# Kernel optimization log

Measured on AMD Instinct MI355X. Metric: run time of the kernel, lower is better.

The kernel has to match this reference:

```python
import jax, jax.numpy as jnp
import numpy as np

N_WIRES = 16
VAR_DEPTH = 2
BATCH = 16


def _param_sizes():
    sizes = []
    n = N_WIRES
    lay = 0
    while n > 1:
        sizes.append(4 * int(np.ceil(N_WIRES / 2 ** lay)) * VAR_DEPTH)
        n = (n + 1) // 2
        lay += 1
    return sizes  # [128, 64, 32, 16]


def _apply_1q(psi, gate, w):
    # psi: (B, 2, ..., 2); gate: (2,2) complex; wire w lives on axis w+1
    psi = jnp.moveaxis(psi, w + 1, -1)
    psi = jnp.einsum('...j,ij->...i', psi, gate)
    return jnp.moveaxis(psi, -1, w + 1)


def _rx(psi, th, w):
    c = jnp.cos(th / 2).astype(jnp.complex64)
    s = jnp.sin(th / 2).astype(jnp.complex64)
    gate = jnp.stack([jnp.stack([c, -1j * s]), jnp.stack([-1j * s, c])])
    return _apply_1q(psi, gate, w)


def _rz(psi, th, w):
    ph = jnp.exp(0.5j * th * jnp.array([-1.0, 1.0], jnp.float32)).astype(jnp.complex64)
    shape = [1] * psi.ndim
    shape[w + 1] = 2
    return psi * ph.reshape(shape)


def _rzz(psi, th, wa, wb):
    # diag(e^{-i t/2}, e^{i t/2}, e^{i t/2}, e^{-i t/2}) -> sign = -1 if bits equal else +1
    sgn = jnp.array([[-1.0, 1.0], [1.0, -1.0]], jnp.float32)
    ph = jnp.exp(0.5j * th * sgn).astype(jnp.complex64)  # symmetric, transpose-safe
    a, b = min(wa, wb) + 1, max(wa, wb) + 1
    shape = [1] * psi.ndim
    shape[a] = 2
    shape[b] = 2
    return psi * ph.reshape(shape)


def _cnot(psi, c, t):
    p0 = jax.lax.slice_in_dim(psi, 0, 1, axis=c + 1)
    p1 = jax.lax.slice_in_dim(psi, 1, 2, axis=c + 1)
    return jnp.concatenate([p0, jnp.flip(p1, axis=t + 1)], axis=c + 1)


def _conv_layer(psi, params, active):
    n = len(active)
    for d in range(VAR_DEPTH):
        for j in range(n):
            base = 4 * j + d * 4 * n
            psi = _rx(psi, params[base + 0], active[j])
            psi = _rz(psi, params[base + 1], active[j])
            psi = _rx(psi, params[base + 2], active[j])
        for bg in (0, 1):
            for j in range(bg, n, 2):
                jn = (j + 1) % n  # ring coupling (wraps last->first)
                base = 4 * j + d * 4 * n
                psi = _rzz(psi, params[base + 3], active[j], active[jn])
    return psi


def _pool(psi, active):
    for j in range(0, len(active), 2):
        if j + 1 < len(active):
            psi = _cnot(psi, active[j], active[j + 1])
    return psi, active[::2]


def _forward(psi, params_list):
    active = list(range(N_WIRES))
    for p in params_list:
        psi = _conv_layer(psi, p, active)
        if len(active) > 1:
            psi, active = _pool(psi, active)
    w = active[0]  # measure Z on the surviving wire (wire 0)
    prob = psi.real ** 2 + psi.imag ** 2
    axes = tuple(a for a in range(1, psi.ndim) if a != w + 1)
    p2 = prob.sum(axis=axes)  # (B, 2)
    return p2[:, 0] - p2[:, 1]


def setup_inputs() -> dict:
    key = jax.random.key(0)
    ks = jax.random.split(key, 8)
    dim = 2 ** N_WIRES
    x_re = jax.random.normal(ks[0], (BATCH, dim), dtype=jnp.float32)
    x_im = jax.random.normal(ks[1], (BATCH, dim), dtype=jnp.float32)
    nrm = jnp.sqrt(jnp.sum(x_re ** 2 + x_im ** 2, axis=1, keepdims=True))
    x_re = x_re / nrm
    x_im = x_im / nrm
    sizes = _param_sizes()
    two_pi = 2.0 * np.pi
    params = [jax.random.uniform(ks[2 + i], (sizes[i],), dtype=jnp.float32) * two_pi
              for i in range(len(sizes))]
    return {"x_re": x_re, "x_im": x_im,
            "params0": params[0], "params1": params[1],
            "params2": params[2], "params3": params[3]}


def reference(x_re, x_im, params0, params1, params2, params3):
    psi = (x_re + 1j * x_im).astype(jnp.complex64)
    psi = psi.reshape((BATCH,) + (2,) * N_WIRES)
    return _forward(psi, [params0, params1, params2, params3])
```

## Files before the change

### kernel.cpp

```cpp
#include <hip/hip_runtime.h>


#define DEV __device__ __forceinline__

__device__ static const unsigned char G_CP[60] = {
  15,14,13,12,11,10,9,8,7,6,5,4,3,2,1,0,
  15,14,13,12,11,10,9,8,7,6,5,4,3,2,1,0,
  15,13,11,9,7,5,3,1,
  15,13,11,9,7,5,3,1,
  15,11,7,3,
  15,11,7,3,
  15,7,
  15,7
};
__device__ static const unsigned char G_CQ[60] = {
  14,13,12,11,10,9,8,7,6,5,4,3,2,1,0,15,
  14,13,12,11,10,9,8,7,6,5,4,3,2,1,0,15,
  13,11,9,7,5,3,1,15,
  13,11,9,7,5,3,1,15,
  11,7,3,15,
  11,7,3,15,
  7,15,
  7,15
};

DEV float2 F2(float x, float y){ float2 r; r.x = x; r.y = y; return r; }
DEV float2 cmulf(float2 a, float2 b){ return F2(a.x*b.x - a.y*b.y, a.x*b.y + a.y*b.x); }
DEV int swz(int j){ return j ^ ((j>>4)&15) ^ ((j>>8)&15); }

template<int B>
DEV void gate(float2* a, const float* __restrict__ g){
  float2 u00=F2(g[0],g[1]), u01=F2(g[2],g[3]), u10=F2(g[4],g[5]), u11=F2(g[6],g[7]);
  #pragma unroll
  for (int m=0; m<8; m++){
    int i0 = ((m>>B)<<(B+1)) | (m & ((1<<B)-1));
    int i1 = i0 | (1<<B);
    float2 x0=a[i0], x1=a[i1];
    a[i0] = F2(u00.x*x0.x - u00.y*x0.y + u01.x*x1.x - u01.y*x1.y,
               u00.x*x0.y + u00.y*x0.x + u01.x*x1.y + u01.y*x1.x);
    a[i1] = F2(u10.x*x0.x - u10.y*x0.y + u11.x*x1.x - u11.y*x1.y,
               u10.x*x0.y + u10.y*x0.x + u11.x*x1.y + u11.y*x1.x);
  }
}

template<int CB,int TB>
DEV void cnotg(float2* a){
  #pragma unroll
  for (int r=0; r<16; r++){
    if ( ((r>>CB)&1)==1 && ((r>>TB)&1)==0 ){
      float2 tmp = a[r]; a[r] = a[r | (1<<TB)]; a[r | (1<<TB)] = tmp;
    }
  }
}

template<int C0,int N,unsigned M0,unsigned M1,unsigned M2,unsigned M3>
DEV void diag(float2* a, const float* __restrict__ tbl, unsigned Ib){
  const unsigned regmask = M0|M1|M2|M3;
  float2 F0 = F2(1.f, 0.f);
  #pragma unroll
  for (int k=0; k<N; k++){
    const int p = G_CP[C0+k], q = G_CQ[C0+k];
    if ( !(((1u<<p)|(1u<<q)) & regmask) ){
      float c = tbl[480 + 2*(C0+k)], s = tbl[481 + 2*(C0+k)];
      unsigned x = ((Ib>>p) ^ (Ib>>q)) & 1u;
      F0 = cmulf(F0, F2(c, x ? s : -s));
    }
  }
  #pragma unroll
  for (int r=0; r<16; r++){
    unsigned Ir = Ib ^ ((r&1)?M0:0u) ^ ((r&2)?M1:0u) ^ ((r&4)?M2:0u) ^ ((r&8)?M3:0u);
    float2 ph = F0;
    #pragma unroll
    for (int k=0; k<N; k++){
      const int p = G_CP[C0+k], q = G_CQ[C0+k];
      if ( ((1u<<p)|(1u<<q)) & regmask ){
        float c = tbl[480 + 2*(C0+k)], s = tbl[481 + 2*(C0+k)];
        unsigned x = ((Ir>>p) ^ (Ir>>q)) & 1u;
        ph = cmulf(ph, F2(c, x ? s : -s));
      }
    }
    a[r] = cmulf(a[r], ph);
  }
}

__global__ void k_setup(const float* __restrict__ p0, const float* __restrict__ p1,
                        const float* __restrict__ p2, const float* __restrict__ p3,
                        float* __restrict__ tbl){
  int g = threadIdx.x;
  if (g >= 60) return;
  int d, j, n; const float* P;
  if (g < 32)      { n=16; d=(g>>4)&1; j=g&15; P=p0; }
  else if (g < 48) { n=8;  d=(g>>3)&1; j=g&7;  P=p1; }
  else if (g < 56) { n=4;  d=(g>>2)&1; j=g&3;  P=p2; }
  else             { n=2;  d=(g>>1)&1; j=g&1;  P=p3; }
  int base = 4*j + 4*n*d;
  double th0 = P[base+0], th1 = P[base+1], th2 = P[base+2], th3 = P[base+3];
  double c0 = cos(th0*0.5), s0 = sin(th0*0.5);
  double ca = cos(th1*0.5), sa = sin(th1*0.5);
  double c2 = cos(th2*0.5), s2 = sin(th2*0.5);
  double B00r =  ca*c0, B00i = -sa*c0;
  double B01r = -sa*s0, B01i = -ca*s0;
  double B10r =  sa*s0, B10i = -ca*s0;
  double B11r =  ca*c0, B11i =  sa*c0;
  double U00r = c2*B00r + s2*B10i, U00i = c2*B00i - s2*B10r;
  double U01r = c2*B01r + s2*B11i, U01i = c2*B01i - s2*B11r;
  double U10r = s2*B00i + c2*B10r, U10i = -s2*B00r + c2*B10i;
  double U11r = s2*B01i + c2*B11r, U11i = -s2*B01r + c2*B11i;
  float* o = tbl + g*8;
  o[0]=(float)U00r; o[1]=(float)U00i; o[2]=(float)U01r; o[3]=(float)U01i;
  o[4]=(float)U10r; o[5]=(float)U10i; o[6]=(float)U11r; o[7]=(float)U11i;
  tbl[480 + 2*g] = (float)cos(th3*0.5);
  tbl[481 + 2*g] = (float)sin(th3*0.5);
}

__global__ __launch_bounds__(256) void k_pass1(const float* __restrict__ xre, const float* __restrict__ xim,
                                               const float* __restrict__ tbl, float2* __restrict__ st){
  const int t = threadIdx.x;
  const int batch = blockIdx.x >> 4, o = blockIdx.x & 15;
  const unsigned hi = ((unsigned)batch<<16) | ((unsigned)o<<12);
  __shared__ float2 lds[2][4096];
  float2 a[16];
  #pragma unroll
  for (int rh=0; rh<4; rh++){
    unsigned I = hi | ((unsigned)t<<2) | ((unsigned)rh<<10);
    float4 re = *(const float4*)(xre + I);
    float4 im = *(const float4*)(xim + I);
    a[rh*4+0]=F2(re.x,im.x); a[rh*4+1]=F2(re.y,im.y);
    a[rh*4+2]=F2(re.z,im.z); a[rh*4+3]=F2(re.w,im.w);
  }
  gate<0>(a, tbl+15*8); gate<1>(a, tbl+14*8); gate<2>(a, tbl+5*8); gate<3>(a, tbl+4*8);
  #pragma unroll
  for (int r=0;r<16;r++){ int j = (r&3) | (t<<2) | ((r>>2)<<10); lds[0][swz(j)] = a[r]; }
  __syncthreads();
  #pragma unroll
  for (int r=0;r<16;r++){ int j = (t&3) | (r<<2) | ((t>>2)<<6); a[r] = lds[0][swz(j)]; }
  gate<0>(a, tbl+13*8); gate<1>(a, tbl+12*8); gate<2>(a, tbl+11*8); gate<3>(a, tbl+10*8);
  #pragma unroll
  for (int r=0;r<16;r++){ int j = (t&3) | (r<<2) | ((t>>2)<<6); lds[1][swz(j)] = a[r]; }
  __syncthreads();
  #pragma unroll
  for (int r=0;r<16;r++){ int j = (t&63) | (r<<6) | ((t>>6)<<10); a[r] = lds[1][swz(j)]; }
  gate<0>(a, tbl+9*8); gate<1>(a, tbl+8*8); gate<2>(a, tbl+7*8); gate<3>(a, tbl+6*8);
  #pragma unroll
  for (int r=0;r<16;r++){ int j = (t&63) | (r<<6) | ((t>>6)<<10); st[hi | j] = a[r]; }
}

__global__ __launch_bounds__(256) void k_pass2(const float* __restrict__ tbl, float2* __restrict__ st){
  const int t = threadIdx.x;
  const int batch = blockIdx.x >> 4, o = blockIdx.x & 15;
  const unsigned bb = (unsigned)batch<<16;
  __shared__ float2 lds[2][4096];
  float2 a[16];
  #pragma unroll
  for (int r=0;r<16;r++){
    unsigned I = (unsigned)(t&63) | ((unsigned)o<<6) | (((unsigned)(t>>6)&3u)<<10) | ((unsigned)r<<12) | bb;
    a[r] = st[I];
  }
  gate<0>(a, tbl+3*8); gate<1>(a, tbl+2*8); gate<2>(a, tbl+1*8); gate<3>(a, tbl+0*8);
  {
    unsigned Ib = (unsigned)(t&63) | ((unsigned)o<<6) | (((unsigned)(t>>6)&3u)<<10);
    diag<0,16, (1u<<12),(1u<<13),(1u<<14),(1u<<15)>(a, tbl, Ib);
  }
  gate<0>(a, tbl+19*8); gate<1>(a, tbl+18*8); gate<2>(a, tbl+17*8); gate<3>(a, tbl+16*8);
  #pragma unroll
  for (int r=0;r<16;r++){ int j = t | (r<<8); lds[0][swz(j)] = a[r]; }
  __syncthreads();
  #pragma unroll
  for (int r=0;r<16;r++){ int j = r | (t<<4); a[r] = lds[0][swz(j)]; }
  gate<0>(a, tbl+31*8); gate<1>(a, tbl+30*8); gate<2>(a, tbl+29*8); gate<3>(a, tbl+28*8);
  #pragma unroll
  for (int r=0;r<16;r++){ int j = r | (t<<4); lds[1][swz(j)] = a[r]; }
  __syncthreads();
  #pragma unroll
  for (int r=0;r<16;r++){ int j = (t&15) | (r<<4) | ((t>>4)<<8); a[r] = lds[1][swz(j)]; }
  gate<0>(a, tbl+27*8); gate<1>(a, tbl+26*8); gate<2>(a, tbl+21*8); gate<3>(a, tbl+20*8);
  #pragma unroll
  for (int r=0;r<16;r++){
    int j = (t&15) | (r<<4) | ((t>>4)<<8);
    unsigned I = (unsigned)(j&63) | ((unsigned)o<<6) | (((unsigned)j>>6)<<10) | bb;
    st[I] = a[r];
  }
}

__global__ __launch_bounds__(256) void k_pass3(const float* __restrict__ tbl, float2* __restrict__ st){
  const int t = threadIdx.x;
  const int batch = blockIdx.x >> 4, o = blockIdx.x & 15;
  const unsigned hi = ((unsigned)batch<<16) | ((unsigned)o<<12);
  float2 a[16];
  #pragma unroll
  for (int r=0;r<16;r++){ int j = (t&63) | (r<<6) | ((t>>6)<<10); a[r] = st[hi | j]; }
  gate<0>(a, tbl+25*8); gate<1>(a, tbl+24*8); gate<2>(a, tbl+23*8); gate<3>(a, tbl+22*8);
  {
    unsigned Ib = ((unsigned)o<<12) | (unsigned)(t&63) | (((unsigned)t>>6)<<10);
    diag<16,16, (1u<<6),(1u<<7),(1u<<8),(1u<<9)>(a, tbl, Ib);
  }
  #pragma unroll
  for (int r=0;r<16;r++){ int j = (t&63) | (r<<6) | ((t>>6)<<10); st[hi | j] = a[r]; }
}

__global__ __launch_bounds__(256) void k_pass4(const float* __restrict__ tbl, float2* __restrict__ st,
                                               float* __restrict__ out){
  const int t = threadIdx.x;
  const int batch = blockIdx.x >> 4, o = blockIdx.x & 15;
  const unsigned bb = (unsigned)batch<<16;
  const unsigned ohi = ((unsigned)(o&1)<<8) | ((unsigned)(o&2)<<9) | ((unsigned)(o&4)<<10) | ((unsigned)(o&8)<<11);
  __shared__ float2 lds[2][4096];
  float2 a[16];
  const unsigned IbA = (unsigned)t | ohi;
  const unsigned jb0 = (unsigned)(t&1) | ((unsigned)(t&2)<<1) | ((unsigned)(t&4)<<2) | ((unsigned)(t&8)<<3);
  const unsigned IbB = jb0 | (((unsigned)(t>>4)&1u)<<9) | (((unsigned)(t>>5)&1u)<<11)
                           | (((unsigned)(t>>6)&1u)<<13) | (((unsigned)(t>>7)&1u)<<15) | ohi;
  #pragma unroll
  for (int r=0;r<16;r++){
    unsigned Il = (unsigned)t | ohi | ((unsigned)(r&1)<<9) | ((unsigned)(r&2)<<10)
                                    | ((unsigned)(r&4)<<11) | ((unsigned)(r&8)<<12);
    unsigned s1 = Il ^ ((Il & 0xAAAAu) >> 1);
    a[r] = st[bb | s1];
  }
  gate<0>(a, tbl+35*8); gate<1>(a, tbl+34*8); gate<2>(a, tbl+33*8); gate<3>(a, tbl+32*8);
  #pragma unroll
  for (int r=0;r<16;r++){ int j = t | (r<<8); lds[0][swz(j)] = a[r]; }
  __syncthreads();
  #pragma unroll
  for (int r=0;r<16;r++){
    int j = (t&1) | ((r&1)<<1) | ((t&2)<<1) | ((r&2)<<2) | ((t&4)<<2) | ((r&4)<<3)
          | ((t&8)<<3) | ((r&8)<<4) | ((t>>4)<<8);
    a[r] = lds[0][swz(j)];
  }
  gate<0>(a, tbl+39*8); gate<1>(a, tbl+38*8); gate<2>(a, tbl+37*8); gate<3>(a, tbl+36*8);
  diag<32,8, 2u,8u,32u,128u>(a, tbl, IbB);
  gate<0>(a, tbl+47*8); gate<1>(a, tbl+46*8); gate<2>(a, tbl+45*8); gate<3>(a, tbl+44*8);
  #pragma unroll
  for (int r=0;r<16;r++){
    int j = (t&1) | ((r&1)<<1) | ((t&2)<<1) | ((r&2)<<2) | ((t&4)<<2) | ((r&4)<<3)
          | ((t&8)<<3) | ((r&8)<<4) | ((t>>4)<<8);
    lds[1][swz(j)] = a[r];
  }
  __syncthreads();
  #pragma unroll
  for (int r=0;r<16;r++){ int j = t | (r<<8); a[r] = lds[1][swz(j)]; }
  gate<0>(a, tbl+43*8); gate<1>(a, tbl+42*8); gate<2>(a, tbl+41*8); gate<3>(a, tbl+40*8);
  diag<40,8, (1u<<9),(1u<<11),(1u<<13),(1u<<15)>(a, tbl, IbA);
  cnotg<3,2>(a); cnotg<1,0>(a);
  #pragma unroll
  for (int r=0;r<16;r++){ int j = t | (r<<8); lds[0][swz(j)] = a[r]; }
  __syncthreads();
  #pragma unroll
  for (int r=0;r<16;r++){
    int j = (t&1) | ((r&1)<<1) | ((t&2)<<1) | ((r&2)<<2) | ((t&4)<<2) | ((r&4)<<3)
          | ((t&8)<<3) | ((r&8)<<4) | ((t>>4)<<8);
    a[r] = lds[0][swz(j)];
  }
  cnotg<3,2>(a); cnotg<1,0>(a);
  gate<3>(a, tbl+50*8); gate<1>(a, tbl+51*8);
  #pragma unroll
  for (int r=0;r<16;r++){
    int j = (t&1) | ((r&1)<<1) | ((t&2)<<1) | ((r&2)<<2) | ((t&4)<<2) | ((r&4)<<3)
          | ((t&8)<<3) | ((r&8)<<4) | ((t>>4)<<8);
    lds[1][swz(j)] = a[r];
  }
  __syncthreads();
  #pragma unroll
  for (int r=0;r<16;r++){ int j = t | (r<<8); a[r] = lds[1][swz(j)]; }
  gate<3>(a, tbl+48*8); gate<1>(a, tbl+49*8);
  diag<48,4, (1u<<9),(1u<<11),(1u<<13),(1u<<15)>(a, tbl, IbA);
  gate<3>(a, tbl+52*8); gate<1>(a, tbl+53*8);
  #pragma unroll
  for (int r=0;r<16;r++){ int j = t | (r<<8); lds[0][swz(j)] = a[r]; }
  __syncthreads();
  #pragma unroll
  for (int r=0;r<16;r++){
    int j = (t&1) | ((r&1)<<1) | ((t&2)<<1) | ((r&2)<<2) | ((t&4)<<2) | ((r&4)<<3)
          | ((t&8)<<3) | ((r&8)<<4) | ((t>>4)<<8);
    a[r] = lds[0][swz(j)];
  }
  gate<3>(a, tbl+54*8); gate<1>(a, tbl+55*8);
  diag<52,4, 2u,8u,32u,128u>(a, tbl, IbB);
  cnotg<3,1>(a);
  gate<3>(a, tbl+57*8);
  #pragma unroll
  for (int r=0;r<16;r++){
    int j = (t&1) | ((r&1)<<1) | ((t&2)<<1) | ((r&2)<<2) | ((t&4)<<2) | ((r&4)<<3)
          | ((t&8)<<3) | ((r&8)<<4) | ((t>>4)<<8);
    lds[1][swz(j)] = a[r];
  }
  __syncthreads();
  #pragma unroll
  for (int r=0;r<16;r++){ int j = t | (r<<8); a[r] = lds[1][swz(j)]; }
  cnotg<3,1>(a);
  gate<3>(a, tbl+56*8);
  diag<56,2, (1u<<9),(1u<<11),(1u<<13),(1u<<15)>(a, tbl, IbA);
  gate<3>(a, tbl+58*8);
  float s = 0.f;
  #pragma unroll
  for (int r=0;r<16;r++){
    float w = a[r].x*a[r].x + a[r].y*a[r].y;
    s += (r & 8) ? -w : w;
  }
  #pragma unroll
  for (int off=32; off>0; off>>=1) s += __shfl_down(s, off);
  float* red = reinterpret_cast<float*>(lds);
  if ((t & 63) == 0) red[t>>6] = s;
  __syncthreads();
  if (t == 0) atomicAdd(out + batch, red[0]+red[1]+red[2]+red[3]);
}

extern "C" void kernel_launch(void* const* d_in, const int* in_sizes, int n_in,
                              void* d_out, int out_size, void* d_ws, size_t ws_size,
                              hipStream_t stream) {
  const float* xre = (const float*)d_in[0];
  const float* xim = (const float*)d_in[1];
  const float* p0  = (const float*)d_in[2];
  const float* p1  = (const float*)d_in[3];
  const float* p2  = (const float*)d_in[4];
  const float* p3  = (const float*)d_in[5];
  float* out = (float*)d_out;
  float* tbl = (float*)d_ws;
  float2* st = (float2*)((char*)d_ws + 16384);

  hipMemsetAsync(d_out, 0, 16*sizeof(float), stream);
  k_setup<<<1, 64, 0, stream>>>(p0, p1, p2, p3, tbl);
  k_pass1<<<256, 256, 0, stream>>>(xre, xim, tbl, st);
  k_pass2<<<256, 256, 0, stream>>>(tbl, st);
  k_pass3<<<256, 256, 0, stream>>>(tbl, st);
  k_pass4<<<256, 256, 0, stream>>>(tbl, st, out);
}
```

Before: 129.3 us.

## Retile state-vector passes to 1024-amplitude blocks with 8 registers per thread

Switches every pass from 4096-amplitude tiles (256 threads, 16 amplitudes each) to 1024-amplitude tiles (128 threads, 8 amplitudes each), launching 1024 blocks instead of 256. The gate, CNOT and diagonal phase schedule is redistributed across passes with new index maps and an adjusted LDS swizzle. The output memset is folded into the setup kernel. The aim is more blocks across the CUs and lower LDS and register use per block, at the cost of more LDS shuffle rounds and barriers per pass.

```diff
diff --git a/kernel.cpp b/kernel.cpp
--- a/kernel.cpp
+++ b/kernel.cpp
@@ -2,6 +2,7 @@
 
 
 #define DEV __device__ __forceinline__
+#define TB(i) (tbl + (i)*8)
 
 __device__ static const unsigned char G_CP[60] = {
   15,14,13,12,11,10,9,8,7,6,5,4,3,2,1,0,
@@ -26,36 +27,36 @@
 
 DEV float2 F2(float x, float y){ float2 r; r.x = x; r.y = y; return r; }
 DEV float2 cmulf(float2 a, float2 b){ return F2(a.x*b.x - a.y*b.y, a.x*b.y + a.y*b.x); }
-DEV int swz(int j){ return j ^ ((j>>4)&15) ^ ((j>>8)&15); }
+DEV int swz(int j){ return j ^ ((j>>4)&15) ^ ((j>>6)&15); }
 
 template<int B>
-DEV void gate(float2* a, const float* __restrict__ g){
-  float2 u00=F2(g[0],g[1]), u01=F2(g[2],g[3]), u10=F2(g[4],g[5]), u11=F2(g[6],g[7]);
-  #pragma unroll
-  for (int m=0; m<8; m++){
+DEV void gate8(float2* a, const float* __restrict__ g){
+  float u00r=g[0],u00i=g[1],u01r=g[2],u01i=g[3],u10r=g[4],u10i=g[5],u11r=g[6],u11i=g[7];
+  #pragma unroll
+  for (int m=0; m<4; m++){
     int i0 = ((m>>B)<<(B+1)) | (m & ((1<<B)-1));
     int i1 = i0 | (1<<B);
     float2 x0=a[i0], x1=a[i1];
-    a[i0] = F2(u00.x*x0.x - u00.y*x0.y + u01.x*x1.x - u01.y*x1.y,
-               u00.x*x0.y + u00.y*x0.x + u01.x*x1.y + u01.y*x1.x);
-    a[i1] = F2(u10.x*x0.x - u10.y*x0.y + u11.x*x1.x - u11.y*x1.y,
-               u10.x*x0.y + u10.y*x0.x + u11.x*x1.y + u11.y*x1.x);
+    a[i0] = F2(u00r*x0.x - u00i*x0.y + u01r*x1.x - u01i*x1.y,
+               u00r*x0.y + u00i*x0.x + u01r*x1.y + u01i*x1.x);
+    a[i1] = F2(u10r*x0.x - u10i*x0.y + u11r*x1.x - u11i*x1.y,
+               u10r*x0.y + u10i*x0.x + u11r*x1.y + u11i*x1.x);
   }
 }
 
 template<int CB,int TB>
-DEV void cnotg(float2* a){
-  #pragma unroll
-  for (int r=0; r<16; r++){
+DEV void cnot8(float2* a){
+  #pragma unroll
+  for (int r=0; r<8; r++){
     if ( ((r>>CB)&1)==1 && ((r>>TB)&1)==0 ){
       float2 tmp = a[r]; a[r] = a[r | (1<<TB)]; a[r | (1<<TB)] = tmp;
     }
   }
 }
 
-template<int C0,int N,unsigned M0,unsigned M1,unsigned M2,unsigned M3>
-DEV void diag(float2* a, const float* __restrict__ tbl, unsigned Ib){
-  const unsigned regmask = M0|M1|M2|M3;
+template<int C0,int N,unsigned M0,unsigned M1,unsigned M2>
+DEV void diag8(float2* a, const float* __restrict__ tbl, unsigned Ib){
+  const unsigned regmask = M0|M1|M2;
   float2 F0 = F2(1.f, 0.f);
   #pragma unroll
   for (int k=0; k<N; k++){
@@ -67,8 +68,8 @@
     }
   }
   #pragma unroll
-  for (int r=0; r<16; r++){
-    unsigned Ir = Ib ^ ((r&1)?M0:0u) ^ ((r&2)?M1:0u) ^ ((r&4)?M2:0u) ^ ((r&8)?M3:0u);
+  for (int r=0; r<8; r++){
+    unsigned Ir = Ib ^ ((r&1)?M0:0u) ^ ((r&2)?M1:0u) ^ ((r&4)?M2:0u);
     float2 ph = F0;
     #pragma unroll
     for (int k=0; k<N; k++){
@@ -85,8 +86,9 @@
 
 __global__ void k_setup(const float* __restrict__ p0, const float* __restrict__ p1,
                         const float* __restrict__ p2, const float* __restrict__ p3,
-                        float* __restrict__ tbl){
+                        float* __restrict__ tbl, float* __restrict__ out){
   int g = threadIdx.x;
+  if (g < 16) out[g] = 0.f;
   if (g >= 60) return;
   int d, j, n; const float* P;
   if (g < 32)      { n=16; d=(g>>4)&1; j=g&15; P=p0; }
@@ -113,196 +115,218 @@
   tbl[481 + 2*g] = (float)sin(th3*0.5);
 }
 
-__global__ __launch_bounds__(256) void k_pass1(const float* __restrict__ xre, const float* __restrict__ xim,
+__global__ __launch_bounds__(128) void k_pass1(const float* __restrict__ xre, const float* __restrict__ xim,
                                                const float* __restrict__ tbl, float2* __restrict__ st){
   const int t = threadIdx.x;
-  const int batch = blockIdx.x >> 4, o = blockIdx.x & 15;
-  const unsigned hi = ((unsigned)batch<<16) | ((unsigned)o<<12);
-  __shared__ float2 lds[2][4096];
-  float2 a[16];
-  #pragma unroll
-  for (int rh=0; rh<4; rh++){
-    unsigned I = hi | ((unsigned)t<<2) | ((unsigned)rh<<10);
-    float4 re = *(const float4*)(xre + I);
-    float4 im = *(const float4*)(xim + I);
-    a[rh*4+0]=F2(re.x,im.x); a[rh*4+1]=F2(re.y,im.y);
-    a[rh*4+2]=F2(re.z,im.z); a[rh*4+3]=F2(re.w,im.w);
-  }
-  gate<0>(a, tbl+15*8); gate<1>(a, tbl+14*8); gate<2>(a, tbl+5*8); gate<3>(a, tbl+4*8);
-  #pragma unroll
-  for (int r=0;r<16;r++){ int j = (r&3) | (t<<2) | ((r>>2)<<10); lds[0][swz(j)] = a[r]; }
-  __syncthreads();
-  #pragma unroll
-  for (int r=0;r<16;r++){ int j = (t&3) | (r<<2) | ((t>>2)<<6); a[r] = lds[0][swz(j)]; }
-  gate<0>(a, tbl+13*8); gate<1>(a, tbl+12*8); gate<2>(a, tbl+11*8); gate<3>(a, tbl+10*8);
-  #pragma unroll
-  for (int r=0;r<16;r++){ int j = (t&3) | (r<<2) | ((t>>2)<<6); lds[1][swz(j)] = a[r]; }
-  __syncthreads();
-  #pragma unroll
-  for (int r=0;r<16;r++){ int j = (t&63) | (r<<6) | ((t>>6)<<10); a[r] = lds[1][swz(j)]; }
-  gate<0>(a, tbl+9*8); gate<1>(a, tbl+8*8); gate<2>(a, tbl+7*8); gate<3>(a, tbl+6*8);
-  #pragma unroll
-  for (int r=0;r<16;r++){ int j = (t&63) | (r<<6) | ((t>>6)<<10); st[hi | j] = a[r]; }
-}
-
-__global__ __launch_bounds__(256) void k_pass2(const float* __restrict__ tbl, float2* __restrict__ st){
+  const int batch = blockIdx.x >> 6, o = blockIdx.x & 63;
+  const unsigned hi = ((unsigned)batch<<16) | ((unsigned)o<<10);
+  __shared__ float2 lds[2][1024];
+  float2 a[8];
+  {
+    unsigned base = hi | ((unsigned)t<<3);
+    float4 r0 = *(const float4*)(xre+base), r1 = *(const float4*)(xre+base+4);
+    float4 i0 = *(const float4*)(xim+base), i1 = *(const float4*)(xim+base+4);
+    a[0]=F2(r0.x,i0.x); a[1]=F2(r0.y,i0.y); a[2]=F2(r0.z,i0.z); a[3]=F2(r0.w,i0.w);
+    a[4]=F2(r1.x,i1.x); a[5]=F2(r1.y,i1.y); a[6]=F2(r1.z,i1.z); a[7]=F2(r1.w,i1.w);
+  }
+  gate8<0>(a, TB(15)); gate8<1>(a, TB(14)); gate8<2>(a, TB(13));
+  #pragma unroll
+  for (int r=0;r<8;r++) lds[0][swz(r | (t<<3))] = a[r];
+  __syncthreads();
+  #pragma unroll
+  for (int r=0;r<8;r++) a[r] = lds[0][swz((t&7) | (r<<3) | ((t>>3)<<6))];
+  gate8<0>(a, TB(12)); gate8<1>(a, TB(11)); gate8<2>(a, TB(10));
+  #pragma unroll
+  for (int r=0;r<8;r++) lds[1][swz((t&7) | (r<<3) | ((t>>3)<<6))] = a[r];
+  __syncthreads();
+  #pragma unroll
+  for (int r=0;r<8;r++) a[r] = lds[1][swz((t&63) | (r<<6) | ((t>>6)<<9))];
+  gate8<0>(a, TB(9)); gate8<1>(a, TB(8)); gate8<2>(a, TB(7));
+  #pragma unroll
+  for (int r=0;r<8;r++) lds[0][swz((t&63) | (r<<6) | ((t>>6)<<9))] = a[r];
+  __syncthreads();
+  #pragma unroll
+  for (int r=0;r<8;r++) a[r] = lds[0][swz(t | (r<<7))];
+  gate8<2>(a, TB(6));
+  #pragma unroll
+  for (int r=0;r<8;r++) st[hi | (unsigned)(t | (r<<7))] = a[r];
+}
+
+DEV unsigned p2I(int j, int o){ return (unsigned)((j&15) | (o<<4) | ((j>>4)<<10)); }
+
+__global__ __launch_bounds__(128) void k_pass2(const float* __restrict__ tbl, float2* __restrict__ st){
   const int t = threadIdx.x;
-  const int batch = blockIdx.x >> 4, o = blockIdx.x & 15;
+  const int batch = blockIdx.x >> 6, o = blockIdx.x & 63;
   const unsigned bb = (unsigned)batch<<16;
-  __shared__ float2 lds[2][4096];
-  float2 a[16];
-  #pragma unroll
-  for (int r=0;r<16;r++){
-    unsigned I = (unsigned)(t&63) | ((unsigned)o<<6) | (((unsigned)(t>>6)&3u)<<10) | ((unsigned)r<<12) | bb;
-    a[r] = st[I];
-  }
-  gate<0>(a, tbl+3*8); gate<1>(a, tbl+2*8); gate<2>(a, tbl+1*8); gate<3>(a, tbl+0*8);
-  {
-    unsigned Ib = (unsigned)(t&63) | ((unsigned)o<<6) | (((unsigned)(t>>6)&3u)<<10);
-    diag<0,16, (1u<<12),(1u<<13),(1u<<14),(1u<<15)>(a, tbl, Ib);
-  }
-  gate<0>(a, tbl+19*8); gate<1>(a, tbl+18*8); gate<2>(a, tbl+17*8); gate<3>(a, tbl+16*8);
-  #pragma unroll
-  for (int r=0;r<16;r++){ int j = t | (r<<8); lds[0][swz(j)] = a[r]; }
-  __syncthreads();
-  #pragma unroll
-  for (int r=0;r<16;r++){ int j = r | (t<<4); a[r] = lds[0][swz(j)]; }
-  gate<0>(a, tbl+31*8); gate<1>(a, tbl+30*8); gate<2>(a, tbl+29*8); gate<3>(a, tbl+28*8);
-  #pragma unroll
-  for (int r=0;r<16;r++){ int j = r | (t<<4); lds[1][swz(j)] = a[r]; }
-  __syncthreads();
-  #pragma unroll
-  for (int r=0;r<16;r++){ int j = (t&15) | (r<<4) | ((t>>4)<<8); a[r] = lds[1][swz(j)]; }
-  gate<0>(a, tbl+27*8); gate<1>(a, tbl+26*8); gate<2>(a, tbl+21*8); gate<3>(a, tbl+20*8);
-  #pragma unroll
-  for (int r=0;r<16;r++){
-    int j = (t&15) | (r<<4) | ((t>>4)<<8);
-    unsigned I = (unsigned)(j&63) | ((unsigned)o<<6) | (((unsigned)j>>6)<<10) | bb;
-    st[I] = a[r];
-  }
-}
-
-__global__ __launch_bounds__(256) void k_pass3(const float* __restrict__ tbl, float2* __restrict__ st){
+  __shared__ float2 lds[2][1024];
+  float2 a[8];
+  #pragma unroll
+  for (int r=0;r<8;r++) a[r] = st[bb | p2I(t | (r<<7), o)];
+  gate8<0>(a, TB(2)); gate8<1>(a, TB(1)); gate8<2>(a, TB(0));
+  #pragma unroll
+  for (int r=0;r<8;r++) lds[0][swz(t | (r<<7))] = a[r];
+  __syncthreads();
+  #pragma unroll
+  for (int r=0;r<8;r++) a[r] = lds[0][swz((t&15) | (r<<4) | ((t>>4)<<7))];
+  gate8<0>(a, TB(5)); gate8<1>(a, TB(4)); gate8<2>(a, TB(3));
+  diag8<0,16, (1u<<10),(1u<<11),(1u<<12)>(a, tbl, p2I((t&15) | ((t>>4)<<7), o));
+  gate8<0>(a, TB(21)); gate8<1>(a, TB(20)); gate8<2>(a, TB(19));
+  #pragma unroll
+  for (int r=0;r<8;r++) lds[1][swz((t&15) | (r<<4) | ((t>>4)<<7))] = a[r];
+  __syncthreads();
+  #pragma unroll
+  for (int r=0;r<8;r++) a[r] = lds[1][swz(t | (r<<7))];
+  gate8<0>(a, TB(18)); gate8<1>(a, TB(17)); gate8<2>(a, TB(16));
+  #pragma unroll
+  for (int r=0;r<8;r++) lds[0][swz(t | (r<<7))] = a[r];
+  __syncthreads();
+  #pragma unroll
+  for (int r=0;r<8;r++) a[r] = lds[0][swz(r | (t<<3))];
+  gate8<0>(a, TB(31)); gate8<1>(a, TB(30)); gate8<2>(a, TB(29));
+  #pragma unroll
+  for (int r=0;r<8;r++) lds[1][swz(r | (t<<3))] = a[r];
+  __syncthreads();
+  #pragma unroll
+  for (int r=0;r<8;r++) a[r] = lds[1][swz((t&7) | (r<<3) | ((t>>3)<<6))];
+  gate8<0>(a, TB(28));
+  #pragma unroll
+  for (int r=0;r<8;r++) st[bb | p2I((t&7) | (r<<3) | ((t>>3)<<6), o)] = a[r];
+}
+
+__global__ __launch_bounds__(128) void k_pass3(const float* __restrict__ tbl, float2* __restrict__ st){
   const int t = threadIdx.x;
-  const int batch = blockIdx.x >> 4, o = blockIdx.x & 15;
-  const unsigned hi = ((unsigned)batch<<16) | ((unsigned)o<<12);
-  float2 a[16];
-  #pragma unroll
-  for (int r=0;r<16;r++){ int j = (t&63) | (r<<6) | ((t>>6)<<10); a[r] = st[hi | j]; }
-  gate<0>(a, tbl+25*8); gate<1>(a, tbl+24*8); gate<2>(a, tbl+23*8); gate<3>(a, tbl+22*8);
-  {
-    unsigned Ib = ((unsigned)o<<12) | (unsigned)(t&63) | (((unsigned)t>>6)<<10);
-    diag<16,16, (1u<<6),(1u<<7),(1u<<8),(1u<<9)>(a, tbl, Ib);
-  }
-  #pragma unroll
-  for (int r=0;r<16;r++){ int j = (t&63) | (r<<6) | ((t>>6)<<10); st[hi | j] = a[r]; }
-}
-
-__global__ __launch_bounds__(256) void k_pass4(const float* __restrict__ tbl, float2* __restrict__ st,
+  const int batch = blockIdx.x >> 6, o = blockIdx.x & 63;
+  const unsigned hi = ((unsigned)batch<<16) | ((unsigned)o<<10);
+  __shared__ float2 lds[2][1024];
+  float2 a[8];
+  #pragma unroll
+  for (int r=0;r<8;r++) a[r] = st[hi | (unsigned)((t&15) | (r<<4) | ((t>>4)<<7))];
+  gate8<0>(a, TB(27)); gate8<1>(a, TB(26)); gate8<2>(a, TB(25));
+  #pragma unroll
+  for (int r=0;r<8;r++) lds[0][swz((t&15) | (r<<4) | ((t>>4)<<7))] = a[r];
+  __syncthreads();
+  #pragma unroll
+  for (int r=0;r<8;r++) a[r] = lds[0][swz(t | (r<<7))];
+  gate8<0>(a, TB(24)); gate8<1>(a, TB(23)); gate8<2>(a, TB(22));
+  diag8<16,16, (1u<<7),(1u<<8),(1u<<9)>(a, tbl, (unsigned)t | ((unsigned)o<<10));
+  #pragma unroll
+  for (int r=0;r<8;r++) st[hi | (unsigned)(t | (r<<7))] = a[r];
+}
+
+DEV unsigned p4I(int j, unsigned og){
+  return (unsigned)( (j&15) | (((j>>4)&1)<<5) | (((j>>5)&1)<<7) | (((j>>6)&1)<<9)
+                   | (((j>>7)&1)<<11) | (((j>>8)&1)<<13) | (((j>>9)&1)<<15) ) | og;
+}
+DEV int p4_jA(int t,int r){ return t | (r<<7); }
+DEV int p4_jB(int t,int r){ return (t&15) | (r<<4) | ((t>>4)<<7); }
+DEV int p4_jC(int t,int r){ return (t&1) | ((r&1)<<1) | (((t>>1)&1)<<2) | (((r>>1)&1)<<3)
+                                  | (((t>>2)&1)<<4) | (((r>>2)&1)<<5) | ((t>>3)<<6); }
+DEV int p4_jD(int t,int r){ return (t&15) | ((r&1)<<4) | (((t>>4)&1)<<5) | (((r>>1)&1)<<6)
+                                  | (((t>>5)&1)<<7) | (((r>>2)&1)<<8) | ((t>>6)<<9); }
+DEV int p4_jF(int t,int r){ return (t&63) | ((r&1)<<6) | (((r>>1)&1)<<7) | (((t>>6)&1)<<8) | ((r>>2)<<9); }
+DEV int p4_jG(int t,int r){ return (t&15) | ((r&3)<<4) | (((t>>4)&7)<<6) | ((r>>2)<<9); }
+DEV int p4_jJ(int t,int r){ return (t&7) | ((r&1)<<3) | (((t>>3)&1)<<4) | (((r>>1)&1)<<5)
+                                  | (((t>>4)&7)<<6) | ((r>>2)<<9); }
+
+__global__ __launch_bounds__(128) void k_pass4(const float* __restrict__ tbl, float2* __restrict__ st,
                                                float* __restrict__ out){
   const int t = threadIdx.x;
-  const int batch = blockIdx.x >> 4, o = blockIdx.x & 15;
+  const int batch = blockIdx.x >> 6, o = blockIdx.x & 63;
   const unsigned bb = (unsigned)batch<<16;
-  const unsigned ohi = ((unsigned)(o&1)<<8) | ((unsigned)(o&2)<<9) | ((unsigned)(o&4)<<10) | ((unsigned)(o&8)<<11);
-  __shared__ float2 lds[2][4096];
-  float2 a[16];
-  const unsigned IbA = (unsigned)t | ohi;
-  const unsigned jb0 = (unsigned)(t&1) | ((unsigned)(t&2)<<1) | ((unsigned)(t&4)<<2) | ((unsigned)(t&8)<<3);
-  const unsigned IbB = jb0 | (((unsigned)(t>>4)&1u)<<9) | (((unsigned)(t>>5)&1u)<<11)
-                           | (((unsigned)(t>>6)&1u)<<13) | (((unsigned)(t>>7)&1u)<<15) | ohi;
-  #pragma unroll
-  for (int r=0;r<16;r++){
-    unsigned Il = (unsigned)t | ohi | ((unsigned)(r&1)<<9) | ((unsigned)(r&2)<<10)
-                                    | ((unsigned)(r&4)<<11) | ((unsigned)(r&8)<<12);
-    unsigned s1 = Il ^ ((Il & 0xAAAAu) >> 1);
+  const unsigned og = ((unsigned)(o&1)<<4) | ((unsigned)(o&2)<<5) | ((unsigned)(o&4)<<6)
+                    | ((unsigned)(o&8)<<7) | ((unsigned)(o&16)<<8) | ((unsigned)(o&32)<<9);
+  __shared__ float2 lds[2][1024];
+  float2 a[8];
+  #pragma unroll
+  for (int r=0;r<8;r++){
+    unsigned I = p4I(p4_jA(t,r), og);
+    unsigned s1 = I ^ ((I & 0xAAAAu) >> 1);
     a[r] = st[bb | s1];
   }
-  gate<0>(a, tbl+35*8); gate<1>(a, tbl+34*8); gate<2>(a, tbl+33*8); gate<3>(a, tbl+32*8);
-  #pragma unroll
-  for (int r=0;r<16;r++){ int j = t | (r<<8); lds[0][swz(j)] = a[r]; }
-  __syncthreads();
-  #pragma unroll
-  for (int r=0;r<16;r++){
-    int j = (t&1) | ((r&1)<<1) | ((t&2)<<1) | ((r&2)<<2) | ((t&4)<<2) | ((r&4)<<3)
-          | ((t&8)<<3) | ((r&8)<<4) | ((t>>4)<<8);
-    a[r] = lds[0][swz(j)];
-  }
-  gate<0>(a, tbl+39*8); gate<1>(a, tbl+38*8); gate<2>(a, tbl+37*8); gate<3>(a, tbl+36*8);
-  diag<32,8, 2u,8u,32u,128u>(a, tbl, IbB);
-  gate<0>(a, tbl+47*8); gate<1>(a, tbl+46*8); gate<2>(a, tbl+45*8); gate<3>(a, tbl+44*8);
-  #pragma unroll
-  for (int r=0;r<16;r++){
-    int j = (t&1) | ((r&1)<<1) | ((t&2)<<1) | ((r&2)<<2) | ((t&4)<<2) | ((r&4)<<3)
-          | ((t&8)<<3) | ((r&8)<<4) | ((t>>4)<<8);
-    lds[1][swz(j)] = a[r];
-  }
-  __syncthreads();
-  #pragma unroll
-  for (int r=0;r<16;r++){ int j = t | (r<<8); a[r] = lds[1][swz(j)]; }
-  gate<0>(a, tbl+43*8); gate<1>(a, tbl+42*8); gate<2>(a, tbl+41*8); gate<3>(a, tbl+40*8);
-  diag<40,8, (1u<<9),(1u<<11),(1u<<13),(1u<<15)>(a, tbl, IbA);
-  cnotg<3,2>(a); cnotg<1,0>(a);
-  #pragma unroll
-  for (int r=0;r<16;r++){ int j = t | (r<<8); lds[0][swz(j)] = a[r]; }
-  __syncthreads();
-  #pragma unroll
-  for (int r=0;r<16;r++){
-    int j = (t&1) | ((r&1)<<1) | ((t&2)<<1) | ((r&2)<<2) | ((t&4)<<2) | ((r&4)<<3)
-          | ((t&8)<<3) | ((r&8)<<4) | ((t>>4)<<8);
-    a[r] = lds[0][swz(j)];
-  }
-  cnotg<3,2>(a); cnotg<1,0>(a);
-  gate<3>(a, tbl+50*8); gate<1>(a, tbl+51*8);
-  #pragma unroll
-  for (int r=0;r<16;r++){
-    int j = (t&1) | ((r&1)<<1) | ((t&2)<<1) | ((r&2)<<2) | ((t&4)<<2) | ((r&4)<<3)
-          | ((t&8)<<3) | ((r&8)<<4) | ((t>>4)<<8);
-    lds[1][swz(j)] = a[r];
-  }
-  __syncthreads();
-  #pragma unroll
-  for (int r=0;r<16;r++){ int j = t | (r<<8); a[r] = lds[1][swz(j)]; }
-  gate<3>(a, tbl+48*8); gate<1>(a, tbl+49*8);
-  diag<48,4, (1u<<9),(1u<<11),(1u<<13),(1u<<15)>(a, tbl, IbA);
-  gate<3>(a, tbl+52*8); gate<1>(a, tbl+53*8);
-  #pragma unroll
-  for (int r=0;r<16;r++){ int j = t | (r<<8); lds[0][swz(j)] = a[r]; }
-  __syncthreads();
-  #pragma unroll
-  for (int r=0;r<16;r++){
-    int j = (t&1) | ((r&1)<<1) | ((t&2)<<1) | ((r&2)<<2) | ((t&4)<<2) | ((r&4)<<3)
-          | ((t&8)<<3) | ((r&8)<<4) | ((t>>4)<<8);
-    a[r] = lds[0][swz(j)];
-  }
-  gate<3>(a, tbl+54*8); gate<1>(a, tbl+55*8);
-  diag<52,4, 2u,8u,32u,128u>(a, tbl, IbB);
-  cnotg<3,1>(a);
-  gate<3>(a, tbl+57*8);
-  #pragma unroll
-  for (int r=0;r<16;r++){
-    int j = (t&1) | ((r&1)<<1) | ((t&2)<<1) | ((r&2)<<2) | ((t&4)<<2) | ((r&4)<<3)
-          | ((t&8)<<3) | ((r&8)<<4) | ((t>>4)<<8);
-    lds[1][swz(j)] = a[r];
-  }
-  __syncthreads();
-  #pragma unroll
-  for (int r=0;r<16;r++){ int j = t | (r<<8); a[r] = lds[1][swz(j)]; }
-  cnotg<3,1>(a);
-  gate<3>(a, tbl+56*8);
-  diag<56,2, (1u<<9),(1u<<11),(1u<<13),(1u<<15)>(a, tbl, IbA);
-  gate<3>(a, tbl+58*8);
+  gate8<0>(a, TB(34)); gate8<1>(a, TB(33)); gate8<2>(a, TB(32));
+  #pragma unroll
+  for (int r=0;r<8;r++) lds[0][swz(p4_jA(t,r))] = a[r];
+  __syncthreads();
+  #pragma unroll
+  for (int r=0;r<8;r++) a[r] = lds[0][swz(p4_jB(t,r))];
+  gate8<0>(a, TB(37)); gate8<1>(a, TB(36)); gate8<2>(a, TB(35));
+  #pragma unroll
+  for (int r=0;r<8;r++) lds[1][swz(p4_jB(t,r))] = a[r];
+  __syncthreads();
+  #pragma unroll
+  for (int r=0;r<8;r++) a[r] = lds[1][swz(p4_jC(t,r))];
+  gate8<0>(a, TB(39)); gate8<1>(a, TB(38));
+  diag8<32,8, 2u,8u,128u>(a, tbl, p4I(p4_jC(t,0), og));
+  gate8<0>(a, TB(47)); gate8<1>(a, TB(46)); gate8<2>(a, TB(44));
+  #pragma unroll
+  for (int r=0;r<8;r++) lds[0][swz(p4_jC(t,r))] = a[r];
+  __syncthreads();
+  #pragma unroll
+  for (int r=0;r<8;r++) a[r] = lds[0][swz(p4_jD(t,r))];
+  gate8<0>(a, TB(45)); gate8<1>(a, TB(43)); gate8<2>(a, TB(41));
+  #pragma unroll
+  for (int r=0;r<8;r++) lds[1][swz(p4_jD(t,r))] = a[r];
+  __syncthreads();
+  #pragma unroll
+  for (int r=0;r<8;r++) a[r] = lds[1][swz(p4_jA(t,r))];
+  gate8<0>(a, TB(42)); gate8<2>(a, TB(40));
+  diag8<40,8, (1u<<11),(1u<<13),(1u<<15)>(a, tbl, p4I(p4_jA(t,0), og));
+  cnot8<2,1>(a);
+  gate8<2>(a, TB(48));
+  #pragma unroll
+  for (int r=0;r<8;r++) lds[0][swz(p4_jA(t,r))] = a[r];
+  __syncthreads();
+  #pragma unroll
+  for (int r=0;r<8;r++) a[r] = lds[0][swz(p4_jF(t,r))];
+  cnot8<1,0>(a);
+  gate8<1>(a, TB(49));
+  #pragma unroll
+  for (int r=0;r<8;r++) lds[1][swz(p4_jF(t,r))] = a[r];
+  __syncthreads();
+  #pragma unroll
+  for (int r=0;r<8;r++) a[r] = lds[1][swz(p4_jG(t,r))];
+  cnot8<1,0>(a);
+  gate8<1>(a, TB(50));
+  #pragma unroll
+  for (int r=0;r<8;r++) lds[0][swz(p4_jG(t,r))] = a[r];
+  __syncthreads();
+  #pragma unroll
+  for (int r=0;r<8;r++) a[r] = lds[0][swz(p4_jC(t,r))];
+  cnot8<1,0>(a);
+  gate8<1>(a, TB(51));
+  diag8<48,4, 2u,8u,128u>(a, tbl, p4I(p4_jC(t,0), og));
+  gate8<1>(a, TB(55)); gate8<2>(a, TB(54));
+  #pragma unroll
+  for (int r=0;r<8;r++) lds[1][swz(p4_jC(t,r))] = a[r];
+  __syncthreads();
+  #pragma unroll
+  for (int r=0;r<8;r++) a[r] = lds[1][swz(p4_jA(t,r))];
+  gate8<0>(a, TB(53)); gate8<2>(a, TB(52));
+  diag8<52,4, (1u<<11),(1u<<13),(1u<<15)>(a, tbl, p4I(p4_jA(t,0), og));
+  cnot8<2,0>(a);
+  gate8<2>(a, TB(56));
+  #pragma unroll
+  for (int r=0;r<8;r++) lds[0][swz(p4_jA(t,r))] = a[r];
+  __syncthreads();
+  #pragma unroll
+  for (int r=0;r<8;r++) a[r] = lds[0][swz(p4_jJ(t,r))];
+  cnot8<1,0>(a);
+  gate8<1>(a, TB(57));
+  diag8<56,2, 8u,128u,(1u<<15)>(a, tbl, p4I(p4_jJ(t,0), og));
+  gate8<2>(a, TB(58));
   float s = 0.f;
   #pragma unroll
-  for (int r=0;r<16;r++){
+  for (int r=0;r<8;r++){
     float w = a[r].x*a[r].x + a[r].y*a[r].y;
-    s += (r & 8) ? -w : w;
+    s += (r & 4) ? -w : w;
   }
   #pragma unroll
   for (int off=32; off>0; off>>=1) s += __shfl_down(s, off);
+  __syncthreads();
   float* red = reinterpret_cast<float*>(lds);
   if ((t & 63) == 0) red[t>>6] = s;
   __syncthreads();
-  if (t == 0) atomicAdd(out + batch, red[0]+red[1]+red[2]+red[3]);
+  if (t == 0) atomicAdd(out + batch, red[0] + red[1]);
 }
 
 extern "C" void kernel_launch(void* const* d_in, const int* in_sizes, int n_in,
@@ -318,10 +342,9 @@
   float* tbl = (float*)d_ws;
   float2* st = (float2*)((char*)d_ws + 16384);
 
-  hipMemsetAsync(d_out, 0, 16*sizeof(float), stream);
-  k_setup<<<1, 64, 0, stream>>>(p0, p1, p2, p3, tbl);
-  k_pass1<<<256, 256, 0, stream>>>(xre, xim, tbl, st);
-  k_pass2<<<256, 256, 0, stream>>>(tbl, st);
-  k_pass3<<<256, 256, 0, stream>>>(tbl, st);
-  k_pass4<<<256, 256, 0, stream>>>(tbl, st, out);
-}
+  k_setup<<<1, 64, 0, stream>>>(p0, p1, p2, p3, tbl, out);
+  k_pass1<<<1024, 128, 0, stream>>>(xre, xim, tbl, st);
+  k_pass2<<<1024, 128, 0, stream>>>(tbl, st);
+  k_pass3<<<1024, 128, 0, stream>>>(tbl, st);
+  k_pass4<<<1024, 128, 0, stream>>>(tbl, st, out);
+}
```

After: 122.8 us. 1.05x faster.
